# Optimization experiments

Measured on AMD Instinct MI355X. Metric: run time of the kernel, lower is better.

Reference implementation:

```python
import jax, jax.numpy as jnp
import numpy as np

PI = np.pi
B, T, L = 1024, 16, 16
XDIM = T * L * 2  # 512
H = 1024
NSTEPS = 10
EPS = 0.1
BETA = 4.0


def convert_to_angle(x):
    # wrap to [-pi, pi)
    return jnp.mod(x + PI, 2.0 * PI) - PI


def setup_inputs() -> dict:
    key = jax.random.key(0)
    ks = jax.random.split(key, 32)
    inp = {
        'x': jax.random.uniform(ks[0], (B, XDIM), jnp.float32, -PI, PI),
        'v': jax.random.normal(ks[1], (2, B, XDIM), jnp.float32),
        'eps': jnp.full((1,), EPS, jnp.float32),
        'beta': jnp.full((1,), BETA, jnp.float32),
        'rand_dir': jax.random.uniform(ks[2], (B,), jnp.float32),
        'rand_accept': jax.random.uniform(ks[3], (B,), jnp.float32),
        'masks': ((jnp.arange(XDIM)[None, :] % 2) == (jnp.arange(NSTEPS)[:, None] % 2)).astype(jnp.float32),
    }
    names = ['W1', 'b1', 'W2', 'b2', 'Ws', 'bs', 'Wt', 'bt', 'Wq', 'bq']
    shapes = [(2 * XDIM, H), (H,), (H, H), (H,), (H, XDIM), (XDIM,), (H, XDIM), (XDIM,), (H, XDIM), (XDIM,)]
    i = 4
    for pre in ['x', 'v']:
        for n, s in zip(names, shapes):
            inp[pre + n] = 0.02 * jax.random.normal(ks[i], s, jnp.float32)
            i += 1
    return inp


def _net(inp, W1, b1, W2, b2, Ws, bs, Wt, bt, Wq, bq):
    h = jnp.tanh(inp @ W1 + b1)
    h = jnp.tanh(h @ W2 + b2)
    S = jnp.tanh(h @ Ws + bs)   # scale
    Tt = h @ Wt + bt            # translation
    Q = jnp.tanh(h @ Wq + bq)   # transformation
    return S, Tt, Q


def _apply_transition(x, v, eps, beta, rand_dir, rand_accept, masks, xparams, vparams):
    eps = eps[0]
    beta_s = beta[0]

    def plaq_sums(xx):
        xl = xx.reshape(-1, T, L, 2)
        return (xl[..., 0] - xl[..., 1]
                - jnp.roll(xl[..., 0], shift=-1, axis=2)
                + jnp.roll(xl[..., 1], shift=-1, axis=1))

    def action(xx):  # [B]
        return beta_s * jnp.sum(1.0 - jnp.cos(plaq_sums(xx)), axis=(1, 2))

    grad_action = jax.grad(lambda xx: jnp.sum(action(xx)))

    def vnet(xx, g):
        return _net(jnp.concatenate([xx, g], axis=-1), *vparams)

    def xnet(vv, mx):
        return _net(jnp.concatenate([vv, mx], axis=-1), *xparams)

    def update_v_fwd(xx, vv, ld):
        g = grad_action(xx)
        S, Tt, Q = vnet(xx, g)
        sc = 0.5 * eps * S
        vv = vv * jnp.exp(sc) - 0.5 * eps * (g * jnp.exp(eps * Q) + Tt)
        return vv, ld + jnp.sum(sc, axis=1)

    def update_x_fwd(xx, vv, m, ld):
        mb = 1.0 - m
        S, Tt, Q = xnet(vv, m * xx)
        sc = eps * S
        xnew = m * xx + mb * (xx * jnp.exp(sc) + eps * (vv * jnp.exp(eps * Q) + Tt))
        return convert_to_angle(xnew), ld + jnp.sum(mb * sc, axis=1)

    def fwd_step(carry, m):
        xx, vv, ld = carry
        vv, ld = update_v_fwd(xx, vv, ld)
        xx, ld = update_x_fwd(xx, vv, m, ld)
        xx, ld = update_x_fwd(xx, vv, 1.0 - m, ld)
        vv, ld = update_v_fwd(xx, vv, ld)
        return (xx, vv, ld), None

    def update_v_bwd(xx, vv, ld):
        g = grad_action(xx)
        S, Tt, Q = vnet(xx, g)
        sc = -0.5 * eps * S
        vv = jnp.exp(sc) * (vv + 0.5 * eps * (g * jnp.exp(eps * Q) + Tt))
        return vv, ld + jnp.sum(sc, axis=1)

    def update_x_bwd(xx, vv, m, ld):
        mb = 1.0 - m
        S, Tt, Q = xnet(vv, m * xx)
        sc = -eps * S
        xnew = m * xx + mb * jnp.exp(sc) * (xx - eps * (vv * jnp.exp(eps * Q) + Tt))
        return convert_to_angle(xnew), ld + jnp.sum(mb * sc, axis=1)

    def bwd_step(carry, m):
        xx, vv, ld = carry
        vv, ld = update_v_bwd(xx, vv, ld)
        xx, ld = update_x_bwd(xx, vv, 1.0 - m, ld)  # invert forward's 2nd x-update first
        xx, ld = update_x_bwd(xx, vv, m, ld)
        vv, ld = update_v_bwd(xx, vv, ld)
        return (xx, vv, ld), None

    zero = jnp.zeros(x.shape[0], x.dtype)
    (xf, vf, ldf), _ = jax.lax.scan(fwd_step, (x, v[0], zero), masks)
    (xb, vb, ldb), _ = jax.lax.scan(bwd_step, (x, v[1], zero), jnp.flip(masks, 0))

    mf = (rand_dir < 0.5).astype(x.dtype)
    mb_ = 1.0 - mf
    v_init = v[0] * mf[:, None] + v[1] * mb_[:, None]
    x_prop = xf * mf[:, None] + xb * mb_[:, None]
    v_prop = vf * mf[:, None] + vb * mb_[:, None]
    sld_prop = ldf * mf + ldb * mb_

    h_init = action(x) + 0.5 * jnp.sum(v_init ** 2, axis=1)
    h_prop = action(x_prop) + 0.5 * jnp.sum(v_prop ** 2, axis=1)
    px = jnp.exp(jnp.minimum(h_init - h_prop + sld_prop, 0.0))

    ma = (rand_accept < px).astype(x.dtype)
    x_out = convert_to_angle(ma[:, None] * x_prop + (1.0 - ma)[:, None] * x)
    sld_out = ma * sld_prop
    return x_out, px, sld_out


def reference(x, v, eps, beta, rand_dir, rand_accept, masks,
              xW1, xb1, xW2, xb2, xWs, xbs, xWt, xbt, xWq, xbq,
              vW1, vb1, vW2, vb2, vWs, vbs, vWt, vbt, vWq, vbq):
    xparams = (xW1, xb1, xW2, xb2, xWs, xbs, xWt, xbt, xWq, xbq)
    vparams = (vW1, vb1, vW2, vb2, vWs, vbs, vWt, vbt, vWq, vbq)
    return _apply_transition(x, v, eps, beta, rand_dir, rand_accept, masks, xparams, vparams)
```

## Files before the change

kernel.cpp:

```cpp
#include <hip/hip_runtime.h>
#include <math.h>

namespace {

constexpr int NB = 1024;
constexpr int ND = 512;
constexpr int NH = 1024;
constexpr int NM = 2048;
constexpr int KTOT = 1024;

typedef __attribute__((ext_vector_type(8))) short short8;
typedef __attribute__((ext_vector_type(4))) float floatx4;

__device__ __forceinline__ unsigned short f2bf(float f) {
  unsigned int u = __float_as_uint(f);
  unsigned int r = (u + 0x7FFFu + ((u >> 16) & 1u)) >> 16;
  return (unsigned short)r;
}
__device__ __forceinline__ float bf2f(unsigned short h) {
  return __uint_as_float(((unsigned int)h) << 16);
}
__device__ __forceinline__ void split2(float f, unsigned short& h, unsigned short& l) {
  h = f2bf(f);
  l = f2bf(f - bf2f(h));
}

__device__ __forceinline__ float wrap_angle(float x) {
  const float PI_F = 3.14159265358979323846f;
  const float TWO_PI = 6.28318530717958647692f;
  const float INV_TWO_PI = 0.15915494309189533577f;
  float y = x + PI_F;
  float r = y - TWO_PI * floorf(y * INV_TWO_PI);
  return r - PI_F;
}

__global__ __launch_bounds__(256) void tcvt_k(
    const float* __restrict__ in, int N,
    unsigned short* __restrict__ out_hi, unsigned short* __restrict__ out_lo,
    int rowoff)
{
  __shared__ float t[32][33];
  int tx = threadIdx.x, ty = threadIdx.y;
  int k0 = blockIdx.y * 32, n0 = blockIdx.x * 32;
#pragma unroll
  for (int i = 0; i < 4; ++i)
    t[ty * 4 + i][tx] = in[(size_t)(k0 + ty * 4 + i) * N + n0 + tx];
  __syncthreads();
#pragma unroll
  for (int i = 0; i < 4; ++i) {
    float f = t[tx][ty * 4 + i];
    unsigned short h, l;
    split2(f, h, l);
    size_t idx = (size_t)(rowoff + n0 + ty * 4 + i) * KTOT + k0 + tx;
    out_hi[idx] = h;
    out_lo[idx] = l;
  }
}

template <int ACT, int OUTF32>
__global__ __launch_bounds__(256) void gemm_k(
    const unsigned short* __restrict__ A0h, const unsigned short* __restrict__ A0l,
    const unsigned short* __restrict__ A1h, const unsigned short* __restrict__ A1l,
    int sA,
    const unsigned short* __restrict__ Bh, const unsigned short* __restrict__ Bl,
    const float* __restrict__ bias,
    float* __restrict__ outf,
    unsigned short* __restrict__ oh, unsigned short* __restrict__ ol,
    int ldo)
{
  __shared__ __align__(16) unsigned short As_h[64 * 64];
  __shared__ __align__(16) unsigned short As_l[64 * 64];
  __shared__ __align__(16) unsigned short Bs_h[64 * 64];
  __shared__ __align__(16) unsigned short Bs_l[64 * 64];

  const int tid = threadIdx.x, lane = tid & 63, w = tid >> 6;
  const int row0 = blockIdx.y * 64, col0 = blockIdx.x * 64;

  const int arl = tid >> 2;
  const int s2 = (tid & 3) * 2;
  const int wofs0 = arl * 64 + ((s2 ^ (arl & 7)) * 8);
  const int wofs1 = arl * 64 + (((s2 + 1) ^ (arl & 7)) * 8);

  short8 rah0, rah1, ral0, ral1, rbh0, rbh1, rbl0, rbl1;

  auto load_regs = [&](int kt) {
    const unsigned short* Ah = (kt >= 8) ? A1h : A0h;
    const unsigned short* Al = (kt >= 8) ? A1l : A0l;
    const int ka = (kt & 7) * 64 + s2 * 8;
    size_t ao = (size_t)(row0 + arl) * sA + ka;
    rah0 = *reinterpret_cast<const short8*>(Ah + ao);
    rah1 = *reinterpret_cast<const short8*>(Ah + ao + 8);
    ral0 = *reinterpret_cast<const short8*>(Al + ao);
    ral1 = *reinterpret_cast<const short8*>(Al + ao + 8);
    const int kb = kt * 64 + s2 * 8;
    size_t bo = (size_t)(col0 + arl) * KTOT + kb;
    rbh0 = *reinterpret_cast<const short8*>(Bh + bo);
    rbh1 = *reinterpret_cast<const short8*>(Bh + bo + 8);
    rbl0 = *reinterpret_cast<const short8*>(Bl + bo);
    rbl1 = *reinterpret_cast<const short8*>(Bl + bo + 8);
  };

  const int wr = w >> 1, wc = w & 1;
  const int rsel = lane & 15, ksel = lane >> 4;
  int arow[2], brow[2];
#pragma unroll
  for (int i = 0; i < 2; ++i) {
    arow[i] = wr * 32 + i * 16 + rsel;
    brow[i] = wc * 32 + i * 16 + rsel;
  }

  floatx4 acc[2][2];
#pragma unroll
  for (int i = 0; i < 2; ++i)
#pragma unroll
    for (int j = 0; j < 2; ++j) acc[i][j] = (floatx4)0.f;

  load_regs(0);

  for (int kt = 0; kt < 16; ++kt) {
    __syncthreads();
    *reinterpret_cast<short8*>(As_h + wofs0) = rah0;
    *reinterpret_cast<short8*>(As_h + wofs1) = rah1;
    *reinterpret_cast<short8*>(As_l + wofs0) = ral0;
    *reinterpret_cast<short8*>(As_l + wofs1) = ral1;
    *reinterpret_cast<short8*>(Bs_h + wofs0) = rbh0;
    *reinterpret_cast<short8*>(Bs_h + wofs1) = rbh1;
    *reinterpret_cast<short8*>(Bs_l + wofs0) = rbl0;
    *reinterpret_cast<short8*>(Bs_l + wofs1) = rbl1;
    __syncthreads();
    if (kt < 15) load_regs(kt + 1);
#pragma unroll
    for (int ks = 0; ks < 2; ++ks) {
      const int kgr = ks * 4 + ksel;
      short8 ah8[2], al8[2], bh8[2], bl8[2];
#pragma unroll
      for (int i = 0; i < 2; ++i) {
        int ao = arow[i] * 64 + ((kgr ^ (arow[i] & 7)) * 8);
        ah8[i] = *reinterpret_cast<const short8*>(As_h + ao);
        al8[i] = *reinterpret_cast<const short8*>(As_l + ao);
        int bo = brow[i] * 64 + ((kgr ^ (brow[i] & 7)) * 8);
        bh8[i] = *reinterpret_cast<const short8*>(Bs_h + bo);
        bl8[i] = *reinterpret_cast<const short8*>(Bs_l + bo);
      }
      __builtin_amdgcn_s_setprio(1);
#pragma unroll
      for (int i = 0; i < 2; ++i)
#pragma unroll
        for (int j = 0; j < 2; ++j) {
          acc[i][j] = __builtin_amdgcn_mfma_f32_16x16x32_bf16(
              ah8[i], bh8[j], acc[i][j], 0, 0, 0);
          acc[i][j] = __builtin_amdgcn_mfma_f32_16x16x32_bf16(
              ah8[i], bl8[j], acc[i][j], 0, 0, 0);
          acc[i][j] = __builtin_amdgcn_mfma_f32_16x16x32_bf16(
              al8[i], bh8[j], acc[i][j], 0, 0, 0);
        }
      __builtin_amdgcn_s_setprio(0);
    }
  }

#pragma unroll
  for (int i = 0; i < 2; ++i)
#pragma unroll
    for (int j = 0; j < 2; ++j) {
      int gr = row0 + wr * 32 + i * 16 + ksel * 4;
      int gc = col0 + wc * 32 + j * 16 + rsel;
      float bb = bias[gc];
      bool dt = (ACT == 1) || (ACT == 2 && !(gc >= 512 && gc < 1024));
#pragma unroll
      for (int rg = 0; rg < 4; ++rg) {
        float v = acc[i][j][rg] + bb;
        if (dt) v = tanhf(v);
        if constexpr (OUTF32) {
          outf[(size_t)(gr + rg) * ldo + gc] = v;
        } else {
          unsigned short h, l;
          split2(v, h, l);
          oh[(size_t)(gr + rg) * ldo + gc] = h;
          ol[(size_t)(gr + rg) * ldo + gc] = l;
        }
      }
    }
}

__device__ __forceinline__ void grad_from_lds(
    const float* xsh, float* sp, float beta, int row,
    float* __restrict__ g, unsigned short* __restrict__ gh,
    unsigned short* __restrict__ gl)
{
  int s0 = threadIdx.x * 2;
#pragma unroll
  for (int u = 0; u < 2; ++u) {
    int s = s0 + u, tt = s >> 4, l = s & 15;
    float p = xsh[s * 2] - xsh[s * 2 + 1]
            - xsh[(tt * 16 + ((l + 1) & 15)) * 2]
            + xsh[(((tt + 1) & 15) * 16 + l) * 2 + 1];
    sp[s] = sinf(p);
  }
  __syncthreads();
  float* gr = g + (size_t)row * ND;
  unsigned short* ghr = gh + (size_t)row * ND;
  unsigned short* glr = gl + (size_t)row * ND;
#pragma unroll
  for (int u = 0; u < 2; ++u) {
    int s = s0 + u, tt = s >> 4, l = s & 15;
    float g0 = beta * (sp[s] - sp[tt * 16 + ((l - 1) & 15)]);
    float g1 = beta * (sp[((tt - 1) & 15) * 16 + l] - sp[s]);
    gr[s * 2] = g0;
    gr[s * 2 + 1] = g1;
    unsigned short h0, l0, h1v, l1v;
    split2(g0, h0, l0);
    split2(g1, h1v, l1v);
    ghr[s * 2] = h0; glr[s * 2] = l0;
    ghr[s * 2 + 1] = h1v; glr[s * 2 + 1] = l1v;
  }
}

__global__ __launch_bounds__(128) void grad_k(
    const float* __restrict__ xs, const float* __restrict__ betap,
    float* __restrict__ g, unsigned short* __restrict__ gh,
    unsigned short* __restrict__ gl)
{
  __shared__ float xsh[512];
  __shared__ float sp[256];
  int row = blockIdx.x, c = threadIdx.x << 2;
  float4 x4 = *reinterpret_cast<const float4*>(xs + (size_t)row * ND + c);
  xsh[c] = x4.x; xsh[c + 1] = x4.y; xsh[c + 2] = x4.z; xsh[c + 3] = x4.w;
  __syncthreads();
  grad_from_lds(xsh, sp, betap[0], row, g, gh, gl);
}

__global__ __launch_bounds__(128) void init_k(
    const float* __restrict__ x_in, const float* __restrict__ v_in,
    const float* __restrict__ m0F, const float* __restrict__ m0B,
    float* __restrict__ xs, float* __restrict__ vs,
    unsigned short* __restrict__ xh, unsigned short* __restrict__ xl,
    unsigned short* __restrict__ xmh, unsigned short* __restrict__ xml,
    unsigned short* __restrict__ vh, unsigned short* __restrict__ vl,
    float* __restrict__ ld)
{
  int row = blockIdx.x;
  bool fwd = row < NB;
  int c = threadIdx.x << 2;
  size_t off = (size_t)row * ND + c;
  const float* xr = x_in + (size_t)(fwd ? row : row - NB) * ND + c;
  const float* vr = v_in + off;
  const float* mk = (fwd ? m0F : m0B) + c;
  float4 x4 = *reinterpret_cast<const float4*>(xr);
  float4 v4 = *reinterpret_cast<const float4*>(vr);
  float4 m4 = *reinterpret_cast<const float4*>(mk);
  float xx[4] = {x4.x, x4.y, x4.z, x4.w};
  float vv[4] = {v4.x, v4.y, v4.z, v4.w};
  float mm[4] = {m4.x, m4.y, m4.z, m4.w};
  ushort4 xhv, xlv, xmhv, xmlv, vhv, vlv;
  unsigned short* ph = (unsigned short*)&xhv;
  unsigned short* pl = (unsigned short*)&xlv;
  unsigned short* pmh = (unsigned short*)&xmhv;
  unsigned short* pml = (unsigned short*)&xmlv;
  unsigned short* pvh = (unsigned short*)&vhv;
  unsigned short* pvl = (unsigned short*)&vlv;
#pragma unroll
  for (int j = 0; j < 4; ++j) {
    float m = fwd ? mm[j] : 1.f - mm[j];
    split2(xx[j], ph[j], pl[j]);
    split2(m * xx[j], pmh[j], pml[j]);
    split2(vv[j], pvh[j], pvl[j]);
  }
  *reinterpret_cast<float4*>(xs + off) = make_float4(xx[0], xx[1], xx[2], xx[3]);
  *reinterpret_cast<float4*>(vs + off) = make_float4(vv[0], vv[1], vv[2], vv[3]);
  *reinterpret_cast<ushort4*>(xh + off) = xhv;
  *reinterpret_cast<ushort4*>(xl + off) = xlv;
  *reinterpret_cast<ushort4*>(xmh + off) = xmhv;
  *reinterpret_cast<ushort4*>(xml + off) = xmlv;
  *reinterpret_cast<ushort4*>(vh + off) = vhv;
  *reinterpret_cast<ushort4*>(vl + off) = vlv;
  if (threadIdx.x == 0) ld[row] = 0.f;
}

__global__ __launch_bounds__(128) void upd_v_k(
    float* __restrict__ vs, const float* __restrict__ g,
    const float* __restrict__ STQ,
    const float* __restrict__ epsp, float* __restrict__ ld,
    unsigned short* __restrict__ vh, unsigned short* __restrict__ vl,
    int twice)
{
  int row = blockIdx.x;
  bool fwd = row < NB;
  int c = threadIdx.x << 2;
  float eps = epsp[0];
  size_t off = (size_t)row * ND + c;
  const float* sr = STQ + (size_t)row * 1536;
  float4 v4 = *reinterpret_cast<float4*>(vs + off);
  float4 g4 = *reinterpret_cast<const float4*>(g + off);
  float4 S4 = *reinterpret_cast<const float4*>(sr + c);
  float4 T4 = *reinterpret_cast<const float4*>(sr + 512 + c);
  float4 Q4 = *reinterpret_cast<const float4*>(sr + 1024 + c);
  float vv[4] = {v4.x, v4.y, v4.z, v4.w};
  float gg[4] = {g4.x, g4.y, g4.z, g4.w};
  float ss[4] = {S4.x, S4.y, S4.z, S4.w};
  float tt[4] = {T4.x, T4.y, T4.z, T4.w};
  float qq[4] = {Q4.x, Q4.y, Q4.z, Q4.w};
  float scsum = 0.f;
  ushort4 hv, lv;
  unsigned short* ph = (unsigned short*)&hv;
  unsigned short* pl = (unsigned short*)&lv;
#pragma unroll
  for (int j = 0; j < 4; ++j) {
    float sc = (fwd ? 0.5f : -0.5f) * eps * ss[j];
    float F = gg[j] * expf(eps * qq[j]) + tt[j];
    vv[j] = fwd ? vv[j] * expf(sc) - 0.5f * eps * F
                : expf(sc) * (vv[j] + 0.5f * eps * F);
    scsum += sc;
    if (twice) {
      vv[j] = fwd ? vv[j] * expf(sc) - 0.5f * eps * F
                  : expf(sc) * (vv[j] + 0.5f * eps * F);
      scsum += sc;
    }
    split2(vv[j], ph[j], pl[j]);
  }
  *reinterpret_cast<float4*>(vs + off) = make_float4(vv[0], vv[1], vv[2], vv[3]);
  *reinterpret_cast<ushort4*>(vh + off) = hv;
  *reinterpret_cast<ushort4*>(vl + off) = lv;
  for (int o = 32; o > 0; o >>= 1) scsum += __shfl_down(scsum, o);
  __shared__ float part[2];
  if ((threadIdx.x & 63) == 0) part[threadIdx.x >> 6] = scsum;
  __syncthreads();
  if (threadIdx.x == 0) ld[row] += part[0] + part[1];
}

__global__ __launch_bounds__(128) void upd_x_k(
    float* __restrict__ xs, const float* __restrict__ vs,
    const float* __restrict__ STQ,
    const float* __restrict__ maskF, int invF,
    const float* __restrict__ maskB, int invB,
    const float* __restrict__ nmF, int niF,
    const float* __restrict__ nmB, int niB,
    const float* __restrict__ epsp, const float* __restrict__ betap,
    float* __restrict__ g, float* __restrict__ ld,
    unsigned short* __restrict__ xh, unsigned short* __restrict__ xl,
    unsigned short* __restrict__ xmh, unsigned short* __restrict__ xml,
    unsigned short* __restrict__ gh, unsigned short* __restrict__ gl)
{
  __shared__ float xsh[512];
  __shared__ float sp[256];
  int row = blockIdx.x;
  bool fwd = row < NB;
  const float* mk = fwd ? maskF : maskB;
  const float* nmk = fwd ? nmF : nmB;
  int inv = fwd ? invF : invB;
  int ninv = fwd ? niF : niB;
  int c = threadIdx.x << 2;
  float eps = epsp[0];
  size_t off = (size_t)row * ND + c;
  const float* sr = STQ + (size_t)row * 1536;
  float4 x4 = *reinterpret_cast<float4*>(xs + off);
  float4 v4 = *reinterpret_cast<const float4*>(vs + off);
  float4 m4 = *reinterpret_cast<const float4*>(mk + c);
  float4 n4 = *reinterpret_cast<const float4*>(nmk + c);
  float4 S4 = *reinterpret_cast<const float4*>(sr + c);
  float4 T4 = *reinterpret_cast<const float4*>(sr + 512 + c);
  float4 Q4 = *reinterpret_cast<const float4*>(sr + 1024 + c);
  float xx[4] = {x4.x, x4.y, x4.z, x4.w};
  float vv[4] = {v4.x, v4.y, v4.z, v4.w};
  float mm[4] = {m4.x, m4.y, m4.z, m4.w};
  float nn[4] = {n4.x, n4.y, n4.z, n4.w};
  float ss[4] = {S4.x, S4.y, S4.z, S4.w};
  float tt[4] = {T4.x, T4.y, T4.z, T4.w};
  float qq[4] = {Q4.x, Q4.y, Q4.z, Q4.w};
  float scsum = 0.f;
  float xn[4];
  ushort4 hv, lv, mhv, mlv;
  unsigned short* ph = (unsigned short*)&hv;
  unsigned short* pl = (unsigned short*)&lv;
  unsigned short* pmh = (unsigned short*)&mhv;
  unsigned short* pml = (unsigned short*)&mlv;
#pragma unroll
  for (int j = 0; j < 4; ++j) {
    float m = inv ? 1.f - mm[j] : mm[j];
    float mb = 1.f - m;
    float es = eps * ss[j];
    float F = vv[j] * expf(eps * qq[j]) + tt[j];
    float t;
    if (fwd) {
      t = m * xx[j] + mb * (xx[j] * expf(es) + eps * F);
      scsum += mb * es;
    } else {
      t = m * xx[j] + mb * (expf(-es) * (xx[j] - eps * F));
      scsum -= mb * es;
    }
    xn[j] = wrap_angle(t);
    xsh[c + j] = xn[j];
    float nm = ninv ? 1.f - nn[j] : nn[j];
    split2(xn[j], ph[j], pl[j]);
    split2(nm * xn[j], pmh[j], pml[j]);
  }
  *reinterpret_cast<float4*>(xs + off) = make_float4(xn[0], xn[1], xn[2], xn[3]);
  *reinterpret_cast<ushort4*>(xh + off) = hv;
  *reinterpret_cast<ushort4*>(xl + off) = lv;
  *reinterpret_cast<ushort4*>(xmh + off) = mhv;
  *reinterpret_cast<ushort4*>(xml + off) = mlv;
  __syncthreads();
  grad_from_lds(xsh, sp, betap[0], row, g, gh, gl);
  for (int o = 32; o > 0; o >>= 1) scsum += __shfl_down(scsum, o);
  __shared__ float part[2];
  if ((threadIdx.x & 63) == 0) part[threadIdx.x >> 6] = scsum;
  __syncthreads();
  if (threadIdx.x == 0) ld[row] += part[0] + part[1];
}

__global__ __launch_bounds__(256) void finalize_k(
    const float* __restrict__ x_in, const float* __restrict__ v_in,
    const float* __restrict__ xs, const float* __restrict__ vs,
    const float* __restrict__ ld,
    const float* __restrict__ rdir, const float* __restrict__ racc,
    const float* __restrict__ betap,
    float* __restrict__ out_x, float* __restrict__ out_px,
    float* __restrict__ out_sld)
{
  int b = blockIdx.x, t = threadIdx.x;
  bool fwd = rdir[b] < 0.5f;
  int prow = fwd ? b : NB + b;
  const float* xp = xs + (size_t)prow * ND;
  const float* vp = vs + (size_t)prow * ND;
  const float* vi = v_in + (size_t)(fwd ? 0 : NB) * ND + (size_t)b * ND;
  float sld = ld[prow];
  __shared__ float xs0[512], xs1[512];
  const float* xr = x_in + (size_t)b * ND;
  xs0[t] = xr[t]; xs0[t + 256] = xr[t + 256];
  xs1[t] = xp[t]; xs1[t + 256] = xp[t + 256];
  __syncthreads();
  int tt = t >> 4, l = t & 15;
  int i00 = t * 2, i01 = t * 2 + 1;
  int i10 = (tt * 16 + ((l + 1) & 15)) * 2;
  int i11 = (((tt + 1) & 15) * 16 + l) * 2 + 1;
  float p0 = xs0[i00] - xs0[i01] - xs0[i10] + xs0[i11];
  float p1 = xs1[i00] - xs1[i01] - xs1[i10] + xs1[i11];
  float r0 = 1.f - cosf(p0);
  float r1 = 1.f - cosf(p1);
  float a0v = vi[t], a1v = vi[t + 256];
  float b0v = vp[t], b1v = vp[t + 256];
  float svi = a0v * a0v + a1v * a1v;
  float svp = b0v * b0v + b1v * b1v;
  for (int o = 32; o > 0; o >>= 1) {
    r0  += __shfl_down(r0, o);
    r1  += __shfl_down(r1, o);
    svi += __shfl_down(svi, o);
    svp += __shfl_down(svp, o);
  }
  __shared__ float red[4][4];
  if ((t & 63) == 0) {
    int w = t >> 6;
    red[w][0] = r0; red[w][1] = r1; red[w][2] = svi; red[w][3] = svp;
  }
  __syncthreads();
  __shared__ float px_s;
  if (t == 0) {
    float R0 = 0, R1 = 0, SI = 0, SP = 0;
    for (int w = 0; w < 4; ++w) {
      R0 += red[w][0]; R1 += red[w][1]; SI += red[w][2]; SP += red[w][3];
    }
    float beta = betap[0];
    float h_init = beta * R0 + 0.5f * SI;
    float h_prop = beta * R1 + 0.5f * SP;
    px_s = expf(fminf(h_init - h_prop + sld, 0.f));
  }
  __syncthreads();
  float px = px_s;
  bool ma = racc[b] < px;
  float* ox = out_x + (size_t)b * ND;
  ox[t]       = wrap_angle(ma ? xs1[t]       : xs0[t]);
  ox[t + 256] = wrap_angle(ma ? xs1[t + 256] : xs0[t + 256]);
  if (t == 0) {
    out_px[b] = px;
    out_sld[b] = ma ? sld : 0.f;
  }
}

}

extern "C" void kernel_launch(void* const* d_in, const int* in_sizes, int n_in,
                              void* d_out, int out_size, void* d_ws, size_t ws_size,
                              hipStream_t stream)
{
  const float* x_in = (const float*)d_in[0];
  const float* v_in = (const float*)d_in[1];
  const float* epsp = (const float*)d_in[2];
  const float* betap = (const float*)d_in[3];
  const float* rdir = (const float*)d_in[4];
  const float* racc = (const float*)d_in[5];
  const float* masks = (const float*)d_in[6];
  const float* xW1 = (const float*)d_in[7];
  const float* xb1 = (const float*)d_in[8];
  const float* xW2 = (const float*)d_in[9];
  const float* xb2 = (const float*)d_in[10];
  const float* xWs = (const float*)d_in[11];
  const float* xbs = (const float*)d_in[12];
  const float* xWt = (const float*)d_in[13];
  const float* xbt = (const float*)d_in[14];
  const float* xWq = (const float*)d_in[15];
  const float* xbq = (const float*)d_in[16];
  const float* vW1 = (const float*)d_in[17];
  const float* vb1 = (const float*)d_in[18];
  const float* vW2 = (const float*)d_in[19];
  const float* vb2 = (const float*)d_in[20];
  const float* vWs = (const float*)d_in[21];
  const float* vbs = (const float*)d_in[22];
  const float* vWt = (const float*)d_in[23];
  const float* vbt = (const float*)d_in[24];
  const float* vWq = (const float*)d_in[25];
  const float* vbq = (const float*)d_in[26];

  char* base = (char*)d_ws;
  auto alloc = [&](size_t bytes) {
    char* r = base;
    base += (bytes + 255) & ~(size_t)255;
    return r;
  };
  float* xs = (float*)alloc((size_t)NM * ND * 4);
  float* vs = (float*)alloc((size_t)NM * ND * 4);
  float* g  = (float*)alloc((size_t)NM * ND * 4);
  float* ld = (float*)alloc((size_t)NM * 4);
  unsigned short* xh  = (unsigned short*)alloc((size_t)NM * ND * 2);
  unsigned short* xl  = (unsigned short*)alloc((size_t)NM * ND * 2);
  unsigned short* xmh = (unsigned short*)alloc((size_t)NM * ND * 2);
  unsigned short* xml = (unsigned short*)alloc((size_t)NM * ND * 2);
  unsigned short* vh  = (unsigned short*)alloc((size_t)NM * ND * 2);
  unsigned short* vl  = (unsigned short*)alloc((size_t)NM * ND * 2);
  unsigned short* gh  = (unsigned short*)alloc((size_t)NM * ND * 2);
  unsigned short* gl  = (unsigned short*)alloc((size_t)NM * ND * 2);
  unsigned short* h1h = (unsigned short*)alloc((size_t)NM * NH * 2);
  unsigned short* h1l = (unsigned short*)alloc((size_t)NM * NH * 2);
  unsigned short* h2h = (unsigned short*)alloc((size_t)NM * NH * 2);
  unsigned short* h2l = (unsigned short*)alloc((size_t)NM * NH * 2);
  float* STQ = (float*)alloc((size_t)NM * 1536 * 4);
  unsigned short* xW1h = (unsigned short*)alloc((size_t)NH * KTOT * 2);
  unsigned short* xW1l = (unsigned short*)alloc((size_t)NH * KTOT * 2);
  unsigned short* xW2h = (unsigned short*)alloc((size_t)NH * KTOT * 2);
  unsigned short* xW2l = (unsigned short*)alloc((size_t)NH * KTOT * 2);
  unsigned short* xWsh = (unsigned short*)alloc((size_t)1536 * KTOT * 2);
  unsigned short* xWsl = (unsigned short*)alloc((size_t)1536 * KTOT * 2);
  unsigned short* vW1h = (unsigned short*)alloc((size_t)NH * KTOT * 2);
  unsigned short* vW1l = (unsigned short*)alloc((size_t)NH * KTOT * 2);
  unsigned short* vW2h = (unsigned short*)alloc((size_t)NH * KTOT * 2);
  unsigned short* vW2l = (unsigned short*)alloc((size_t)NH * KTOT * 2);
  unsigned short* vWsh = (unsigned short*)alloc((size_t)1536 * KTOT * 2);
  unsigned short* vWsl = (unsigned short*)alloc((size_t)1536 * KTOT * 2);
  float* bstq_x = (float*)alloc(1536 * 4);
  float* bstq_v = (float*)alloc(1536 * 4);

  dim3 tb(32, 8);
  tcvt_k<<<dim3(32, 32), tb, 0, stream>>>(xW1, 1024, xW1h, xW1l, 0);
  tcvt_k<<<dim3(32, 32), tb, 0, stream>>>(xW2, 1024, xW2h, xW2l, 0);
  tcvt_k<<<dim3(16, 32), tb, 0, stream>>>(xWs, 512, xWsh, xWsl, 0);
  tcvt_k<<<dim3(16, 32), tb, 0, stream>>>(xWt, 512, xWsh, xWsl, 512);
  tcvt_k<<<dim3(16, 32), tb, 0, stream>>>(xWq, 512, xWsh, xWsl, 1024);
  tcvt_k<<<dim3(32, 32), tb, 0, stream>>>(vW1, 1024, vW1h, vW1l, 0);
  tcvt_k<<<dim3(32, 32), tb, 0, stream>>>(vW2, 1024, vW2h, vW2l, 0);
  tcvt_k<<<dim3(16, 32), tb, 0, stream>>>(vWs, 512, vWsh, vWsl, 0);
  tcvt_k<<<dim3(16, 32), tb, 0, stream>>>(vWt, 512, vWsh, vWsl, 512);
  tcvt_k<<<dim3(16, 32), tb, 0, stream>>>(vWq, 512, vWsh, vWsl, 1024);
  hipMemcpyAsync(bstq_x,        xbs, 512 * 4, hipMemcpyDeviceToDevice, stream);
  hipMemcpyAsync(bstq_x + 512,  xbt, 512 * 4, hipMemcpyDeviceToDevice, stream);
  hipMemcpyAsync(bstq_x + 1024, xbq, 512 * 4, hipMemcpyDeviceToDevice, stream);
  hipMemcpyAsync(bstq_v,        vbs, 512 * 4, hipMemcpyDeviceToDevice, stream);
  hipMemcpyAsync(bstq_v + 512,  vbt, 512 * 4, hipMemcpyDeviceToDevice, stream);
  hipMemcpyAsync(bstq_v + 1024, vbq, 512 * 4, hipMemcpyDeviceToDevice, stream);

  init_k<<<NM, 128, 0, stream>>>(x_in, v_in, masks, masks + 9 * ND,
                                 xs, vs, xh, xl, xmh, xml, vh, vl, ld);
  grad_k<<<NM, 128, 0, stream>>>(xs, betap, g, gh, gl);

  auto vnet = [&]() {
    gemm_k<1, 0><<<dim3(16, 32), 256, 0, stream>>>(
        xh, xl, gh, gl, 512, vW1h, vW1l, vb1, nullptr, h1h, h1l, NH);
    gemm_k<1, 0><<<dim3(16, 32), 256, 0, stream>>>(
        h1h, h1l, h1h + 512, h1l + 512, 1024, vW2h, vW2l, vb2,
        nullptr, h2h, h2l, NH);
    gemm_k<2, 1><<<dim3(24, 32), 256, 0, stream>>>(
        h2h, h2l, h2h + 512, h2l + 512, 1024, vWsh, vWsl, bstq_v,
        STQ, nullptr, nullptr, 1536);
  };
  auto xnet = [&]() {
    gemm_k<1, 0><<<dim3(16, 32), 256, 0, stream>>>(
        vh, vl, xmh, xml, 512, xW1h, xW1l, xb1, nullptr, h1h, h1l, NH);
    gemm_k<1, 0><<<dim3(16, 32), 256, 0, stream>>>(
        h1h, h1l, h1h + 512, h1l + 512, 1024, xW2h, xW2l, xb2,
        nullptr, h2h, h2l, NH);
    gemm_k<2, 1><<<dim3(24, 32), 256, 0, stream>>>(
        h2h, h2l, h2h + 512, h2l + 512, 1024, xWsh, xWsl, bstq_x,
        STQ, nullptr, nullptr, 1536);
  };

  vnet();
  upd_v_k<<<NM, 128, 0, stream>>>(vs, g, STQ, epsp, ld, vh, vl, 0);
  for (int s = 0; s < 10; ++s) {
    const float* mF = masks + (size_t)s * ND;
    const float* mB = masks + (size_t)(9 - s) * ND;
    const float* mFn = masks + (size_t)((s + 1 < 10) ? s + 1 : 0) * ND;
    const float* mBn = masks + (size_t)((s + 1 < 10) ? 8 - s : 0) * ND;
    xnet();
    upd_x_k<<<NM, 128, 0, stream>>>(xs, vs, STQ, mF, 0, mB, 1, mF, 1, mB, 0,
                                    epsp, betap, g, ld,
                                    xh, xl, xmh, xml, gh, gl);
    xnet();
    upd_x_k<<<NM, 128, 0, stream>>>(xs, vs, STQ, mF, 1, mB, 0, mFn, 0, mBn, 1,
                                    epsp, betap, g, ld,
                                    xh, xl, xmh, xml, gh, gl);
    vnet();
    upd_v_k<<<NM, 128, 0, stream>>>(vs, g, STQ, epsp, ld, vh, vl,
                                    (s < 9) ? 1 : 0);
  }

  float* out_x = (float*)d_out;
  float* out_px = out_x + (size_t)NB * ND;
  float* out_sld = out_px + NB;
  finalize_k<<<NB, 256, 0, stream>>>(x_in, v_in, xs, vs, ld, rdir, racc, betap,
                                     out_x, out_px, out_sld);
}
```

Before: 2.494 ms.

## Load GEMM B fragments directly from global into registers, bypassing LDS

Drops the shared-memory staging of the B (weight) tile. Each wave now loads its MFMA B fragments straight from global memory into double-buffered registers, one k-tile ahead. This cuts LDS writes and reads and halves shared memory use, which may raise occupancy. The cost is more global load traffic, since B is no longer shared between waves with the same column tile, plus extra register pressure.

After: 4.357 ms. 1.75x slower.

```diff
diff --git a/kernel.cpp b/kernel.cpp
--- a/kernel.cpp
+++ b/kernel.cpp
@@ -70,8 +70,6 @@
 {
   __shared__ __align__(16) unsigned short As_h[64 * 64];
   __shared__ __align__(16) unsigned short As_l[64 * 64];
-  __shared__ __align__(16) unsigned short Bs_h[64 * 64];
-  __shared__ __align__(16) unsigned short Bs_l[64 * 64];
 
   const int tid = threadIdx.x, lane = tid & 63, w = tid >> 6;
   const int row0 = blockIdx.y * 64, col0 = blockIdx.x * 64;
@@ -81,9 +79,9 @@
   const int wofs0 = arl * 64 + ((s2 ^ (arl & 7)) * 8);
   const int wofs1 = arl * 64 + (((s2 + 1) ^ (arl & 7)) * 8);
 
-  short8 rah0, rah1, ral0, ral1, rbh0, rbh1, rbl0, rbl1;
-
-  auto load_regs = [&](int kt) {
+  short8 rah0, rah1, ral0, ral1;
+
+  auto loadA_regs = [&](int kt) {
     const unsigned short* Ah = (kt >= 8) ? A1h : A0h;
     const unsigned short* Al = (kt >= 8) ? A1l : A0l;
     const int ka = (kt & 7) * 64 + s2 * 8;
@@ -92,12 +90,6 @@
     rah1 = *reinterpret_cast<const short8*>(Ah + ao + 8);
     ral0 = *reinterpret_cast<const short8*>(Al + ao);
     ral1 = *reinterpret_cast<const short8*>(Al + ao + 8);
-    const int kb = kt * 64 + s2 * 8;
-    size_t bo = (size_t)(col0 + arl) * KTOT + kb;
-    rbh0 = *reinterpret_cast<const short8*>(Bh + bo);
-    rbh1 = *reinterpret_cast<const short8*>(Bh + bo + 8);
-    rbl0 = *reinterpret_cast<const short8*>(Bl + bo);
-    rbl1 = *reinterpret_cast<const short8*>(Bl + bo + 8);
   };
 
   const int wr = w >> 1, wc = w & 1;
@@ -106,8 +98,21 @@
 #pragma unroll
   for (int i = 0; i < 2; ++i) {
     arow[i] = wr * 32 + i * 16 + rsel;
-    brow[i] = wc * 32 + i * 16 + rsel;
-  }
+    brow[i] = col0 + wc * 32 + i * 16 + rsel;
+  }
+
+  short8 bhA[4], blA[4], bhB[4], blB[4];
+
+  auto loadB = [&](int kt, short8* bh, short8* bl) {
+#pragma unroll
+    for (int ks = 0; ks < 2; ++ks)
+#pragma unroll
+      for (int j = 0; j < 2; ++j) {
+        size_t bo = (size_t)brow[j] * KTOT + kt * 64 + (ks * 4 + ksel) * 8;
+        bh[ks * 2 + j] = *reinterpret_cast<const short8*>(Bh + bo);
+        bl[ks * 2 + j] = *reinterpret_cast<const short8*>(Bl + bo);
+      }
+  };
 
   floatx4 acc[2][2];
 #pragma unroll
@@ -115,46 +120,63 @@
 #pragma unroll
     for (int j = 0; j < 2; ++j) acc[i][j] = (floatx4)0.f;
 
-  load_regs(0);
-
-  for (int kt = 0; kt < 16; ++kt) {
-    __syncthreads();
+  auto mfma_phase = [&](const short8* bh, const short8* bl) {
+#pragma unroll
+    for (int ks = 0; ks < 2; ++ks) {
+      const int kgr = ks * 4 + ksel;
+      short8 ah8[2], al8[2];
+#pragma unroll
+      for (int i = 0; i < 2; ++i) {
+        int ao = arow[i] * 64 + ((kgr ^ (arow[i] & 7)) * 8);
+        ah8[i] = *reinterpret_cast<const short8*>(As_h + ao);
+        al8[i] = *reinterpret_cast<const short8*>(As_l + ao);
+      }
+      __builtin_amdgcn_s_setprio(1);
+#pragma unroll
+      for (int i = 0; i < 2; ++i)
+#pragma unroll
+        for (int j = 0; j < 2; ++j) {
+          acc[i][j] = __builtin_amdgcn_mfma_f32_16x16x32_bf16(
+              ah8[i], bh[ks * 2 + j], acc[i][j], 0, 0, 0);
+          acc[i][j] = __builtin_amdgcn_mfma_f32_16x16x32_bf16(
+              ah8[i], bl[ks * 2 + j], acc[i][j], 0, 0, 0);
+          acc[i][j] = __builtin_amdgcn_mfma_f32_16x16x32_bf16(
+              al8[i], bh[ks * 2 + j], acc[i][j], 0, 0, 0);
+        }
+      __builtin_amdgcn_s_setprio(0);
+    }
+  };
+
+  auto store_A = [&]() {
     *reinterpret_cast<short8*>(As_h + wofs0) = rah0;
     *reinterpret_cast<short8*>(As_h + wofs1) = rah1;
     *reinterpret_cast<short8*>(As_l + wofs0) = ral0;
     *reinterpret_cast<short8*>(As_l + wofs1) = ral1;
-    *reinterpret_cast<short8*>(Bs_h + wofs0) = rbh0;
-    *reinterpret_cast<short8*>(Bs_h + wofs1) = rbh1;
-    *reinterpret_cast<short8*>(Bs_l + wofs0) = rbl0;
-    *reinterpret_cast<short8*>(Bs_l + wofs1) = rbl1;
-    __syncthreads();
-    if (kt < 15) load_regs(kt + 1);
-#pragma unroll
-    for (int ks = 0; ks < 2; ++ks) {
-      const int kgr = ks * 4 + ksel;
-      short8 ah8[2], al8[2], bh8[2], bl8[2];
-#pragma unroll
-      for (int i = 0; i < 2; ++i) {
-        int ao = arow[i] * 64 + ((kgr ^ (arow[i] & 7)) * 8);
-        ah8[i] = *reinterpret_cast<const short8*>(As_h + ao);
-        al8[i] = *reinterpret_cast<const short8*>(As_l + ao);
-        int bo = brow[i] * 64 + ((kgr ^ (brow[i] & 7)) * 8);
-        bh8[i] = *reinterpret_cast<const short8*>(Bs_h + bo);
-        bl8[i] = *reinterpret_cast<const short8*>(Bs_l + bo);
+  };
+
+  loadA_regs(0);
+  loadB(0, bhA, blA);
+
+  for (int kt2 = 0; kt2 < 8; ++kt2) {
+    {
+      const int kt = kt2 * 2;
+      __syncthreads();
+      store_A();
+      __syncthreads();
+      loadA_regs(kt + 1);
+      loadB(kt + 1, bhB, blB);
+      mfma_phase(bhA, blA);
+    }
+    {
+      const int kt = kt2 * 2 + 1;
+      __syncthreads();
+      store_A();
+      __syncthreads();
+      if (kt < 15) {
+        loadA_regs(kt + 1);
+        loadB(kt + 1, bhA, blA);
       }
-      __builtin_amdgcn_s_setprio(1);
-#pragma unroll
-      for (int i = 0; i < 2; ++i)
-#pragma unroll
-        for (int j = 0; j < 2; ++j) {
-          acc[i][j] = __builtin_amdgcn_mfma_f32_16x16x32_bf16(
-              ah8[i], bh8[j], acc[i][j], 0, 0, 0);
-          acc[i][j] = __builtin_amdgcn_mfma_f32_16x16x32_bf16(
-              ah8[i], bl8[j], acc[i][j], 0, 0, 0);
-          acc[i][j] = __builtin_amdgcn_mfma_f32_16x16x32_bf16(
-              al8[i], bh8[j], acc[i][j], 0, 0, 0);
-        }
-      __builtin_amdgcn_s_setprio(0);
+      mfma_phase(bhB, blB);
     }
   }
 
```

## Double-buffer LDS tiles in split-bf16 GEMM to halve barriers per k-step

Applied to the files above, without the earlier changes.

The GEMM now keeps two LDS buffers for the hi/lo A and B tiles. Each k-iteration writes the next tile into the spare buffer and issues the global loads for the tile after that, then runs the MFMAs on the current buffer. This leaves one __syncthreads per iteration instead of two, and lets the LDS stores overlap with MFMA work. The cost is that LDS per block doubles to 64KB, which may cut the number of resident blocks per CU.

Measured after the change: 2.563 ms. 1.03x slower.

```diff
diff --git a/kernel.cpp b/kernel.cpp
--- a/kernel.cpp
+++ b/kernel.cpp
@@ -68,10 +68,10 @@
     unsigned short* __restrict__ oh, unsigned short* __restrict__ ol,
     int ldo)
 {
-  __shared__ __align__(16) unsigned short As_h[64 * 64];
-  __shared__ __align__(16) unsigned short As_l[64 * 64];
-  __shared__ __align__(16) unsigned short Bs_h[64 * 64];
-  __shared__ __align__(16) unsigned short Bs_l[64 * 64];
+  __shared__ __align__(16) unsigned short As_h[2][64 * 64];
+  __shared__ __align__(16) unsigned short As_l[2][64 * 64];
+  __shared__ __align__(16) unsigned short Bs_h[2][64 * 64];
+  __shared__ __align__(16) unsigned short Bs_l[2][64 * 64];
 
   const int tid = threadIdx.x, lane = tid & 63, w = tid >> 6;
   const int row0 = blockIdx.y * 64, col0 = blockIdx.x * 64;
@@ -83,7 +83,7 @@
 
   short8 rah0, rah1, ral0, ral1, rbh0, rbh1, rbl0, rbl1;
 
-  auto load_regs = [&](int kt) {
+  auto loadregs = [&](int kt) {
     const unsigned short* Ah = (kt >= 8) ? A1h : A0h;
     const unsigned short* Al = (kt >= 8) ? A1l : A0l;
     const int ka = (kt & 7) * 64 + s2 * 8;
@@ -100,6 +100,17 @@
     rbl1 = *reinterpret_cast<const short8*>(Bl + bo + 8);
   };
 
+  auto store_tile = [&](int buf) {
+    *reinterpret_cast<short8*>(&As_h[buf][wofs0]) = rah0;
+    *reinterpret_cast<short8*>(&As_h[buf][wofs1]) = rah1;
+    *reinterpret_cast<short8*>(&As_l[buf][wofs0]) = ral0;
+    *reinterpret_cast<short8*>(&As_l[buf][wofs1]) = ral1;
+    *reinterpret_cast<short8*>(&Bs_h[buf][wofs0]) = rbh0;
+    *reinterpret_cast<short8*>(&Bs_h[buf][wofs1]) = rbh1;
+    *reinterpret_cast<short8*>(&Bs_l[buf][wofs0]) = rbl0;
+    *reinterpret_cast<short8*>(&Bs_l[buf][wofs1]) = rbl1;
+  };
+
   const int wr = w >> 1, wc = w & 1;
   const int rsel = lane & 15, ksel = lane >> 4;
   int arow[2], brow[2];
@@ -115,20 +126,7 @@
 #pragma unroll
     for (int j = 0; j < 2; ++j) acc[i][j] = (floatx4)0.f;
 
-  load_regs(0);
-
-  for (int kt = 0; kt < 16; ++kt) {
-    __syncthreads();
-    *reinterpret_cast<short8*>(As_h + wofs0) = rah0;
-    *reinterpret_cast<short8*>(As_h + wofs1) = rah1;
-    *reinterpret_cast<short8*>(As_l + wofs0) = ral0;
-    *reinterpret_cast<short8*>(As_l + wofs1) = ral1;
-    *reinterpret_cast<short8*>(Bs_h + wofs0) = rbh0;
-    *reinterpret_cast<short8*>(Bs_h + wofs1) = rbh1;
-    *reinterpret_cast<short8*>(Bs_l + wofs0) = rbl0;
-    *reinterpret_cast<short8*>(Bs_l + wofs1) = rbl1;
-    __syncthreads();
-    if (kt < 15) load_regs(kt + 1);
+  auto mfma_phase = [&](int buf) {
 #pragma unroll
     for (int ks = 0; ks < 2; ++ks) {
       const int kgr = ks * 4 + ksel;
@@ -136,11 +134,11 @@
 #pragma unroll
       for (int i = 0; i < 2; ++i) {
         int ao = arow[i] * 64 + ((kgr ^ (arow[i] & 7)) * 8);
-        ah8[i] = *reinterpret_cast<const short8*>(As_h + ao);
-        al8[i] = *reinterpret_cast<const short8*>(As_l + ao);
+        ah8[i] = *reinterpret_cast<const short8*>(&As_h[buf][ao]);
+        al8[i] = *reinterpret_cast<const short8*>(&As_l[buf][ao]);
         int bo = brow[i] * 64 + ((kgr ^ (brow[i] & 7)) * 8);
-        bh8[i] = *reinterpret_cast<const short8*>(Bs_h + bo);
-        bl8[i] = *reinterpret_cast<const short8*>(Bs_l + bo);
+        bh8[i] = *reinterpret_cast<const short8*>(&Bs_h[buf][bo]);
+        bl8[i] = *reinterpret_cast<const short8*>(&Bs_l[buf][bo]);
       }
       __builtin_amdgcn_s_setprio(1);
 #pragma unroll
@@ -156,6 +154,18 @@
         }
       __builtin_amdgcn_s_setprio(0);
     }
+  };
+
+  loadregs(0);
+  store_tile(0);
+  loadregs(1);
+  __syncthreads();
+
+  for (int kt = 0; kt < 16; ++kt) {
+    if (kt < 15) store_tile((kt + 1) & 1);
+    if (kt < 14) loadregs(kt + 2);
+    mfma_phase(kt & 1);
+    __syncthreads();
   }
 
 #pragma unroll
```
